# Performance work log

Hardware: AMD Instinct MI355X
Metric: run time of the kernel (lower is better)

## Reference

```python
import jax, jax.numpy as jnp
import numpy as np

N = 50000          # num nodes
E = 800000         # num edges
IN_C, HID_C, OUT_C = 128, 256, 256
LN_EPS = 1e-5


def gcn_conv(x, W, b, row, col):
    """PyG GCNConv: h = D^{-1/2}(A+I)D^{-1/2} (x W) + b, self-loops added."""
    h = x @ W                                             # [N, C_out]
    deg = jax.ops.segment_sum(jnp.ones((row.shape[0],), h.dtype), col,
                              num_segments=N) + 1.0        # +1 for self-loop
    dinv = jax.lax.rsqrt(deg)                              # [N]
    msg = h[row] * (dinv[row] * dinv[col])[:, None]        # [E, C_out] gathered msgs
    agg = jax.ops.segment_sum(msg, col, num_segments=N)
    agg = agg + h * (dinv * dinv)[:, None]                 # self-loop contribution
    return agg + b


def layer_norm(x, gamma, beta):
    mu = jnp.mean(x, axis=-1, keepdims=True)
    var = jnp.mean(jnp.square(x - mu), axis=-1, keepdims=True)
    return (x - mu) * jax.lax.rsqrt(var + LN_EPS) * gamma + beta


def setup_inputs() -> dict:
    key = jax.random.key(0)
    ks = jax.random.split(key, 8)
    x = jax.random.normal(ks[0], (N, IN_C), jnp.float32)
    edge_index = jax.random.randint(ks[1], (2, E), 0, N, dtype=jnp.int64)
    W1 = jax.random.normal(ks[2], (IN_C, HID_C), jnp.float32) * (1.0 / np.sqrt(IN_C))
    b1 = jnp.zeros((HID_C,), jnp.float32)
    W2 = jax.random.normal(ks[3], (HID_C, OUT_C), jnp.float32) * (1.0 / np.sqrt(HID_C))
    b2 = jnp.zeros((OUT_C,), jnp.float32)
    ln1_g = jnp.ones((HID_C,), jnp.float32); ln1_b = jnp.zeros((HID_C,), jnp.float32)
    ln2_g = jnp.ones((OUT_C,), jnp.float32); ln2_b = jnp.zeros((OUT_C,), jnp.float32)
    proj_W = jax.random.normal(ks[4], (IN_C, OUT_C), jnp.float32) * (1.0 / np.sqrt(IN_C))
    proj_b = jnp.zeros((OUT_C,), jnp.float32)
    return {"x": x, "edge_index": edge_index, "W1": W1, "b1": b1, "W2": W2,
            "b2": b2, "ln1_g": ln1_g, "ln1_b": ln1_b, "ln2_g": ln2_g,
            "ln2_b": ln2_b, "proj_W": proj_W, "proj_b": proj_b}


def reference(x, edge_index, W1, b1, W2, b2, ln1_g, ln1_b, ln2_g, ln2_b,
              proj_W, proj_b):
    row, col = edge_index[0], edge_index[1]   # messages flow row -> col
    identity = x @ proj_W + proj_b            # self.proj (Linear, in != out)
    h = gcn_conv(x, W1, b1, row, col)
    h = jax.nn.relu(layer_norm(h, ln1_g, ln1_b))   # dropout = identity (eval)
    g = gcn_conv(h, W2, b2, row, col)
    g = layer_norm(g, ln2_g, ln2_b)
    return jax.nn.relu(g + identity)
```

## Files before the change

### kernel.cpp

```cpp
#include <hip/hip_runtime.h>

#define NN 50000
#define NE 800000
#define LN_EPS 1e-5f

using bf16x8 = __attribute__((ext_vector_type(8))) short;
using f32x4  = __attribute__((ext_vector_type(4))) float;

__device__ __forceinline__ float b2f(unsigned short u) {
    union { unsigned int i; float f; } c;
    c.i = ((unsigned int)u) << 16;
    return c.f;
}
__device__ __forceinline__ unsigned short f2b(float f) {
    union { float f; unsigned int i; } c;
    c.f = f;
    const unsigned int i = c.i;
    return (unsigned short)((i + 0x7FFFu + ((i >> 16) & 1u)) >> 16);
}

__global__ __launch_bounds__(256) void cvt_k(const float* __restrict__ X,
                                             short* __restrict__ Xb, int n4) {
    const int i = blockIdx.x * 256 + threadIdx.x;
    if (i >= n4) return;
    const float4 v = ((const float4*)X)[i];
    ushort4 o;
    o.x = f2b(v.x); o.y = f2b(v.y); o.z = f2b(v.z); o.w = f2b(v.w);
    ((ushort4*)Xb)[i] = o;
}

template <int K>
__global__ __launch_bounds__(256) void pack_w_k(const float* __restrict__ W,
                                                short* __restrict__ Wp) {
    constexpr int KB = K / 32;
    const int i = blockIdx.x * 256 + threadIdx.x;
    const int j = i & 7;
    const int l = (i >> 3) & 63;
    const int t = i >> 9;
    const int kb = t % KB;
    const int nt = t / KB;
    const int k = 32 * kb + 8 * (l >> 4) + j;
    const int n = 16 * nt + (l & 15);
    Wp[i] = (short)f2b(W[(size_t)k * 256 + n]);
}

template <int K, bool OUT_BF16>
__global__ __launch_bounds__(256) void gemm_mfma_k(const short* __restrict__ X,
                                                   const short* __restrict__ Wp,
                                                   const float* __restrict__ bias,
                                                   void* __restrict__ Yv) {
    constexpr int KB = K / 32;
    const int lane = threadIdx.x & 63;
    const int wv = threadIdx.x >> 6;
    const int row0 = blockIdx.x * 64 + wv * 16;
    const int r = row0 + (lane & 15);
    const int rc = (r < NN) ? r : (NN - 1);
    const int kof = 8 * (lane >> 4);

    bf16x8 a[KB];
#pragma unroll
    for (int kb = 0; kb < KB; ++kb)
        a[kb] = *(const bf16x8*)(X + (size_t)rc * K + 32 * kb + kof);

    const int orow0 = row0 + (lane >> 4) * 4;
    const int colbase = lane & 15;

    for (int nt = 0; nt < 16; ++nt) {
        f32x4 acc = {0.f, 0.f, 0.f, 0.f};
#pragma unroll
        for (int kb = 0; kb < KB; ++kb) {
            const bf16x8 b = ((const bf16x8*)Wp)[(nt * KB + kb) * 64 + lane];
            acc = __builtin_amdgcn_mfma_f32_16x16x32_bf16(a[kb], b, acc, 0, 0, 0);
        }
        const int col = nt * 16 + colbase;
        const float bv = bias ? bias[col] : 0.f;
#pragma unroll
        for (int rg = 0; rg < 4; ++rg) {
            const int orow = orow0 + rg;
            if (orow < NN) {
                const float v = acc[rg] + bv;
                if (OUT_BF16)
                    ((short*)Yv)[(size_t)orow * 256 + col] = (short)f2b(v);
                else
                    ((float*)Yv)[(size_t)orow * 256 + col] = v;
            }
        }
    }
}

__global__ __launch_bounds__(256) void count_k(const int* __restrict__ col,
                                               int* __restrict__ rowptr) {
    const int e = blockIdx.x * 256 + threadIdx.x;
    if (e < NE) atomicAdd(&rowptr[col[e] + 1], 1);
}

__global__ __launch_bounds__(256) void block_sum_k(const int* __restrict__ p,
                                                   int* __restrict__ psum, int n) {
    __shared__ int sh[256];
    const int t = threadIdx.x;
    const int i = blockIdx.x * 256 + t;
    sh[t] = (i < n) ? p[i] : 0;
    __syncthreads();
#pragma unroll
    for (int off = 128; off > 0; off >>= 1) {
        if (t < off) sh[t] += sh[t + off];
        __syncthreads();
    }
    if (t == 0) psum[blockIdx.x] = sh[0];
}

__global__ __launch_bounds__(256) void scan_apply_k(int* __restrict__ p,
                                                    const int* __restrict__ psum,
                                                    int n, int nblk) {
    __shared__ int sh[256];
    const int t = threadIdx.x;
    const int b = blockIdx.x;
    const int i = b * 256 + t;
    sh[t] = (t < b && t < nblk) ? psum[t] : 0;
    __syncthreads();
#pragma unroll
    for (int off = 128; off > 0; off >>= 1) {
        if (t < off) sh[t] += sh[t + off];
        __syncthreads();
    }
    const int carry = sh[0];
    __syncthreads();
    sh[t] = (i < n) ? p[i] : 0;
    __syncthreads();
#pragma unroll
    for (int off = 1; off < 256; off <<= 1) {
        const int u = (t >= off) ? sh[t - off] : 0;
        __syncthreads();
        sh[t] += u;
        __syncthreads();
    }
    if (i < n) p[i] = sh[t] + carry;
}

__global__ __launch_bounds__(256) void dinv_k(const int* __restrict__ rowptr,
                                              float* __restrict__ dinv) {
    const int i = blockIdx.x * 256 + threadIdx.x;
    if (i < NN) dinv[i] = rsqrtf((float)(rowptr[i + 1] - rowptr[i]) + 1.0f);
}

__global__ __launch_bounds__(256) void fill_k(const int* __restrict__ row,
                                              const int* __restrict__ col,
                                              int* __restrict__ rowptr,
                                              int* __restrict__ srcs) {
    const int e = blockIdx.x * 256 + threadIdx.x;
    if (e >= NE) return;
    const int pos = atomicAdd(&rowptr[col[e]], 1);
    srcs[pos] = row[e];
}

template <bool OUT_BF16>
__global__ __launch_bounds__(256) void gather_post_k(
    const short* __restrict__ H, const int* __restrict__ endptr,
    const int* __restrict__ srcs, const float* __restrict__ dinv,
    const float* __restrict__ bias, const float* __restrict__ gamma,
    const float* __restrict__ beta, const float* __restrict__ resid,
    void* __restrict__ outv) {
    const int node = blockIdx.x * 4 + (threadIdx.x >> 6);
    const int lane = threadIdx.x & 63;
    if (node >= NN) return;
    const int start = node ? endptr[node - 1] : 0;
    const int end = endptr[node];

    float a0 = 0.f, a1 = 0.f, a2 = 0.f, a3 = 0.f;
    int j = start;
    for (; j + 1 < end; j += 2) {
        const int r0 = srcs[j];
        const int r1 = srcs[j + 1];
        const float w0 = dinv[r0];
        const float w1 = dinv[r1];
        const ushort4 v0 = ((const ushort4*)(H + (size_t)r0 * 256))[lane];
        const ushort4 v1 = ((const ushort4*)(H + (size_t)r1 * 256))[lane];
        a0 += b2f(v0.x) * w0 + b2f(v1.x) * w1;
        a1 += b2f(v0.y) * w0 + b2f(v1.y) * w1;
        a2 += b2f(v0.z) * w0 + b2f(v1.z) * w1;
        a3 += b2f(v0.w) * w0 + b2f(v1.w) * w1;
    }
    if (j < end) {
        const int r0 = srcs[j];
        const float w0 = dinv[r0];
        const ushort4 v0 = ((const ushort4*)(H + (size_t)r0 * 256))[lane];
        a0 += b2f(v0.x) * w0;
        a1 += b2f(v0.y) * w0;
        a2 += b2f(v0.z) * w0;
        a3 += b2f(v0.w) * w0;
    }

    const float dc = dinv[node];
    const ushort4 h = ((const ushort4*)(H + (size_t)node * 256))[lane];
    const float4 b = ((const float4*)bias)[lane];
    float t0 = (a0 + b2f(h.x) * dc) * dc + b.x;
    float t1 = (a1 + b2f(h.y) * dc) * dc + b.y;
    float t2 = (a2 + b2f(h.z) * dc) * dc + b.z;
    float t3 = (a3 + b2f(h.w) * dc) * dc + b.w;

    float s = t0 + t1 + t2 + t3;
    float q = t0 * t0 + t1 * t1 + t2 * t2 + t3 * t3;
#pragma unroll
    for (int off = 1; off < 64; off <<= 1) {
        s += __shfl_xor(s, off, 64);
        q += __shfl_xor(q, off, 64);
    }
    const float mu = s * (1.f / 256.f);
    const float var = q * (1.f / 256.f) - mu * mu;
    const float rs = rsqrtf(var + LN_EPS);

    const float4 g = ((const float4*)gamma)[lane];
    const float4 be = ((const float4*)beta)[lane];
    t0 = (t0 - mu) * rs * g.x + be.x;
    t1 = (t1 - mu) * rs * g.y + be.y;
    t2 = (t2 - mu) * rs * g.z + be.z;
    t3 = (t3 - mu) * rs * g.w + be.w;

    if (resid) {
        const float4 rv = ((const float4*)(resid + (size_t)node * 256))[lane];
        t0 += rv.x; t1 += rv.y; t2 += rv.z; t3 += rv.w;
    }
    t0 = fmaxf(t0, 0.f); t1 = fmaxf(t1, 0.f);
    t2 = fmaxf(t2, 0.f); t3 = fmaxf(t3, 0.f);

    if (OUT_BF16) {
        ushort4 o;
        o.x = f2b(t0); o.y = f2b(t1); o.z = f2b(t2); o.w = f2b(t3);
        ((ushort4*)outv)[(size_t)node * 64 + lane] = o;
    } else {
        float4 o;
        o.x = t0; o.y = t1; o.z = t2; o.w = t3;
        ((float4*)outv)[(size_t)node * 64 + lane] = o;
    }
}

extern "C" void kernel_launch(void* const* d_in, const int* in_sizes, int n_in,
                              void* d_out, int out_size, void* d_ws, size_t ws_size,
                              hipStream_t stream) {
    const float* x    = (const float*)d_in[0];
    const int*   eidx = (const int*)d_in[1];
    const float* W1   = (const float*)d_in[2];
    const float* b1   = (const float*)d_in[3];
    const float* W2   = (const float*)d_in[4];
    const float* b2   = (const float*)d_in[5];
    const float* ln1g = (const float*)d_in[6];
    const float* ln1b = (const float*)d_in[7];
    const float* ln2g = (const float*)d_in[8];
    const float* ln2b = (const float*)d_in[9];
    const float* pW   = (const float*)d_in[10];
    const float* pb   = (const float*)d_in[11];

    const int* row = eidx;
    const int* col = eidx + NE;
    float* out = (float*)d_out;

    short* xb     = (short*)d_ws;
    short* A      = xb + (size_t)NN * 128;
    short* Bb     = A + (size_t)NN * 256;
    float* dinv   = (float*)(Bb + (size_t)NN * 256);
    int*   rowptr = (int*)(dinv + NN);
    int*   psum   = rowptr + NN + 4;
    int*   srcs   = psum + 256;
    short* Wp1    = (short*)(srcs + NE);
    short* Wp2    = Wp1 + 128 * 256;
    short* Wpp    = Wp2 + 256 * 256;

    const int nscan = NN + 1;
    const int nblk = (nscan + 255) / 256;

    cvt_k<<<(NN * 128 / 4 + 255) / 256, 256, 0, stream>>>(x, xb, NN * 128 / 4);
    pack_w_k<128><<<128, 256, 0, stream>>>(W1, Wp1);
    pack_w_k<256><<<256, 256, 0, stream>>>(W2, Wp2);
    pack_w_k<128><<<128, 256, 0, stream>>>(pW, Wpp);

    hipMemsetAsync(rowptr, 0, (NN + 4) * sizeof(int), stream);
    count_k<<<(NE + 255) / 256, 256, 0, stream>>>(col, rowptr);
    block_sum_k<<<nblk, 256, 0, stream>>>(rowptr, psum, nscan);
    scan_apply_k<<<nblk, 256, 0, stream>>>(rowptr, psum, nscan, nblk);
    dinv_k<<<(NN + 255) / 256, 256, 0, stream>>>(rowptr, dinv);
    fill_k<<<(NE + 255) / 256, 256, 0, stream>>>(row, col, rowptr, srcs);

    gemm_mfma_k<128, true><<<(NN + 63) / 64, 256, 0, stream>>>(xb, Wp1, nullptr, A);
    gather_post_k<true><<<(NN + 3) / 4, 256, 0, stream>>>(A, rowptr, srcs, dinv,
                                                          b1, ln1g, ln1b, nullptr, Bb);

    gemm_mfma_k<128, false><<<(NN + 63) / 64, 256, 0, stream>>>(xb, Wpp, pb, out);

    gemm_mfma_k<256, true><<<(NN + 63) / 64, 256, 0, stream>>>(Bb, Wp2, nullptr, A);
    gather_post_k<false><<<(NN + 3) / 4, 256, 0, stream>>>(A, rowptr, srcs, dinv,
                                                           b2, ln2g, ln2b, out, out);
}
```

Baseline: 331.9 us.

## Aggregate before transform and fuse GEMM with bias, LayerNorm and projection

Reorders each GCN layer to aggregate first and multiply by the weight afterwards, using linearity. Layer 1 then gathers 128-wide rows of x instead of 256-wide rows of xW. LayerNorm, bias, the residual projection GEMM and ReLU move into the GEMM epilogue, removing the separate projection pass and the fp32 out read-modify-write. In exchange the GEMM keeps 16 accumulator tiles per wave, which raises register pressure and may lower occupancy. Rounding also shifts because aggregated values are rounded to bf16 before the matmul.

```diff
diff --git a/kernel.cpp b/kernel.cpp
--- a/kernel.cpp
+++ b/kernel.cpp
@@ -44,50 +44,6 @@
     Wp[i] = (short)f2b(W[(size_t)k * 256 + n]);
 }
 
-template <int K, bool OUT_BF16>
-__global__ __launch_bounds__(256) void gemm_mfma_k(const short* __restrict__ X,
-                                                   const short* __restrict__ Wp,
-                                                   const float* __restrict__ bias,
-                                                   void* __restrict__ Yv) {
-    constexpr int KB = K / 32;
-    const int lane = threadIdx.x & 63;
-    const int wv = threadIdx.x >> 6;
-    const int row0 = blockIdx.x * 64 + wv * 16;
-    const int r = row0 + (lane & 15);
-    const int rc = (r < NN) ? r : (NN - 1);
-    const int kof = 8 * (lane >> 4);
-
-    bf16x8 a[KB];
-#pragma unroll
-    for (int kb = 0; kb < KB; ++kb)
-        a[kb] = *(const bf16x8*)(X + (size_t)rc * K + 32 * kb + kof);
-
-    const int orow0 = row0 + (lane >> 4) * 4;
-    const int colbase = lane & 15;
-
-    for (int nt = 0; nt < 16; ++nt) {
-        f32x4 acc = {0.f, 0.f, 0.f, 0.f};
-#pragma unroll
-        for (int kb = 0; kb < KB; ++kb) {
-            const bf16x8 b = ((const bf16x8*)Wp)[(nt * KB + kb) * 64 + lane];
-            acc = __builtin_amdgcn_mfma_f32_16x16x32_bf16(a[kb], b, acc, 0, 0, 0);
-        }
-        const int col = nt * 16 + colbase;
-        const float bv = bias ? bias[col] : 0.f;
-#pragma unroll
-        for (int rg = 0; rg < 4; ++rg) {
-            const int orow = orow0 + rg;
-            if (orow < NN) {
-                const float v = acc[rg] + bv;
-                if (OUT_BF16)
-                    ((short*)Yv)[(size_t)orow * 256 + col] = (short)f2b(v);
-                else
-                    ((float*)Yv)[(size_t)orow * 256 + col] = v;
-            }
-        }
-    }
-}
-
 __global__ __launch_bounds__(256) void count_k(const int* __restrict__ col,
                                                int* __restrict__ rowptr) {
     const int e = blockIdx.x * 256 + threadIdx.x;
@@ -153,13 +109,50 @@
     srcs[pos] = row[e];
 }
 
-template <bool OUT_BF16>
-__global__ __launch_bounds__(256) void gather_post_k(
-    const short* __restrict__ H, const int* __restrict__ endptr,
-    const int* __restrict__ srcs, const float* __restrict__ dinv,
-    const float* __restrict__ bias, const float* __restrict__ gamma,
-    const float* __restrict__ beta, const float* __restrict__ resid,
-    void* __restrict__ outv) {
+__global__ __launch_bounds__(256) void gather1_k(const short* __restrict__ X,
+                                                 const int* __restrict__ endptr,
+                                                 const int* __restrict__ srcs,
+                                                 const float* __restrict__ dinv,
+                                                 short* __restrict__ A1) {
+    const int node = blockIdx.x * 4 + (threadIdx.x >> 6);
+    const int lane = threadIdx.x & 63;
+    if (node >= NN) return;
+    const int start = node ? endptr[node - 1] : 0;
+    const int end = endptr[node];
+
+    float a0 = 0.f, a1 = 0.f;
+    int j = start;
+    for (; j + 1 < end; j += 2) {
+        const int r0 = srcs[j];
+        const int r1 = srcs[j + 1];
+        const float w0 = dinv[r0];
+        const float w1 = dinv[r1];
+        const ushort2 v0 = ((const ushort2*)(X + (size_t)r0 * 128))[lane];
+        const ushort2 v1 = ((const ushort2*)(X + (size_t)r1 * 128))[lane];
+        a0 += b2f(v0.x) * w0 + b2f(v1.x) * w1;
+        a1 += b2f(v0.y) * w0 + b2f(v1.y) * w1;
+    }
+    if (j < end) {
+        const int r0 = srcs[j];
+        const float w0 = dinv[r0];
+        const ushort2 v0 = ((const ushort2*)(X + (size_t)r0 * 128))[lane];
+        a0 += b2f(v0.x) * w0;
+        a1 += b2f(v0.y) * w0;
+    }
+    const float dc = dinv[node];
+    const ushort2 h = ((const ushort2*)(X + (size_t)node * 128))[lane];
+    a0 = (a0 + b2f(h.x) * dc) * dc;
+    a1 = (a1 + b2f(h.y) * dc) * dc;
+    ushort2 o;
+    o.x = f2b(a0); o.y = f2b(a1);
+    ((ushort2*)A1)[(size_t)node * 64 + lane] = o;
+}
+
+__global__ __launch_bounds__(256) void gather2_k(const short* __restrict__ H,
+                                                 const int* __restrict__ endptr,
+                                                 const int* __restrict__ srcs,
+                                                 const float* __restrict__ dinv,
+                                                 short* __restrict__ agg) {
     const int node = blockIdx.x * 4 + (threadIdx.x >> 6);
     const int lane = threadIdx.x & 63;
     if (node >= NN) return;
@@ -189,48 +182,114 @@
         a2 += b2f(v0.z) * w0;
         a3 += b2f(v0.w) * w0;
     }
-
     const float dc = dinv[node];
     const ushort4 h = ((const ushort4*)(H + (size_t)node * 256))[lane];
-    const float4 b = ((const float4*)bias)[lane];
-    float t0 = (a0 + b2f(h.x) * dc) * dc + b.x;
-    float t1 = (a1 + b2f(h.y) * dc) * dc + b.y;
-    float t2 = (a2 + b2f(h.z) * dc) * dc + b.z;
-    float t3 = (a3 + b2f(h.w) * dc) * dc + b.w;
-
-    float s = t0 + t1 + t2 + t3;
-    float q = t0 * t0 + t1 * t1 + t2 * t2 + t3 * t3;
-#pragma unroll
-    for (int off = 1; off < 64; off <<= 1) {
-        s += __shfl_xor(s, off, 64);
-        q += __shfl_xor(q, off, 64);
-    }
-    const float mu = s * (1.f / 256.f);
-    const float var = q * (1.f / 256.f) - mu * mu;
-    const float rs = rsqrtf(var + LN_EPS);
-
-    const float4 g = ((const float4*)gamma)[lane];
-    const float4 be = ((const float4*)beta)[lane];
-    t0 = (t0 - mu) * rs * g.x + be.x;
-    t1 = (t1 - mu) * rs * g.y + be.y;
-    t2 = (t2 - mu) * rs * g.z + be.z;
-    t3 = (t3 - mu) * rs * g.w + be.w;
-
-    if (resid) {
-        const float4 rv = ((const float4*)(resid + (size_t)node * 256))[lane];
-        t0 += rv.x; t1 += rv.y; t2 += rv.z; t3 += rv.w;
-    }
-    t0 = fmaxf(t0, 0.f); t1 = fmaxf(t1, 0.f);
-    t2 = fmaxf(t2, 0.f); t3 = fmaxf(t3, 0.f);
-
-    if (OUT_BF16) {
-        ushort4 o;
-        o.x = f2b(t0); o.y = f2b(t1); o.z = f2b(t2); o.w = f2b(t3);
-        ((ushort4*)outv)[(size_t)node * 64 + lane] = o;
-    } else {
-        float4 o;
-        o.x = t0; o.y = t1; o.z = t2; o.w = t3;
-        ((float4*)outv)[(size_t)node * 64 + lane] = o;
+    ushort4 o;
+    o.x = f2b((a0 + b2f(h.x) * dc) * dc);
+    o.y = f2b((a1 + b2f(h.y) * dc) * dc);
+    o.z = f2b((a2 + b2f(h.z) * dc) * dc);
+    o.w = f2b((a3 + b2f(h.w) * dc) * dc);
+    ((ushort4*)agg)[(size_t)node * 64 + lane] = o;
+}
+
+template <int K, bool PROJ, bool OUT_BF16>
+__global__ __launch_bounds__(256) void gemm_ln_k(
+    const short* __restrict__ X, const short* __restrict__ Wp,
+    const float* __restrict__ bias, const float* __restrict__ gamma,
+    const float* __restrict__ beta, const short* __restrict__ Xp,
+    const short* __restrict__ Wpp, const float* __restrict__ pbias,
+    void* __restrict__ Yv) {
+    constexpr int KB = K / 32;
+    const int lane = threadIdx.x & 63;
+    const int wv = threadIdx.x >> 6;
+    const int row0 = blockIdx.x * 64 + wv * 16;
+    const int r = row0 + (lane & 15);
+    const int rc = (r < NN) ? r : (NN - 1);
+    const int kof = 8 * (lane >> 4);
+    const int colbase = lane & 15;
+
+    bf16x8 a[KB];
+#pragma unroll
+    for (int kb = 0; kb < KB; ++kb)
+        a[kb] = *(const bf16x8*)(X + (size_t)rc * K + 32 * kb + kof);
+
+    f32x4 acc[16];
+#pragma unroll
+    for (int nt = 0; nt < 16; ++nt) {
+        f32x4 c = {0.f, 0.f, 0.f, 0.f};
+#pragma unroll
+        for (int kb = 0; kb < KB; ++kb) {
+            const bf16x8 b = ((const bf16x8*)Wp)[(nt * KB + kb) * 64 + lane];
+            c = __builtin_amdgcn_mfma_f32_16x16x32_bf16(a[kb], b, c, 0, 0, 0);
+        }
+        acc[nt] = c;
+    }
+
+    float s[4] = {0.f, 0.f, 0.f, 0.f};
+    float q[4] = {0.f, 0.f, 0.f, 0.f};
+#pragma unroll
+    for (int nt = 0; nt < 16; ++nt) {
+        const float bv = bias[nt * 16 + colbase];
+#pragma unroll
+        for (int rg = 0; rg < 4; ++rg) {
+            const float v = acc[nt][rg] + bv;
+            acc[nt][rg] = v;
+            s[rg] += v;
+            q[rg] += v * v;
+        }
+    }
+#pragma unroll
+    for (int off = 1; off < 16; off <<= 1) {
+#pragma unroll
+        for (int rg = 0; rg < 4; ++rg) {
+            s[rg] += __shfl_xor(s[rg], off, 64);
+            q[rg] += __shfl_xor(q[rg], off, 64);
+        }
+    }
+    float mu[4], rsd[4];
+#pragma unroll
+    for (int rg = 0; rg < 4; ++rg) {
+        mu[rg] = s[rg] * (1.f / 256.f);
+        const float var = q[rg] * (1.f / 256.f) - mu[rg] * mu[rg];
+        rsd[rg] = rsqrtf(var + LN_EPS);
+    }
+
+    bf16x8 ap[4];
+    if (PROJ) {
+#pragma unroll
+        for (int kb = 0; kb < 4; ++kb)
+            ap[kb] = *(const bf16x8*)(Xp + (size_t)rc * 128 + 32 * kb + kof);
+    }
+
+    const int orow0 = row0 + (lane >> 4) * 4;
+#pragma unroll
+    for (int nt = 0; nt < 16; ++nt) {
+        const int col = nt * 16 + colbase;
+        const float g = gamma[col];
+        const float be = beta[col];
+        f32x4 pid = {0.f, 0.f, 0.f, 0.f};
+        float pbv = 0.f;
+        if (PROJ) {
+#pragma unroll
+            for (int kb = 0; kb < 4; ++kb) {
+                const bf16x8 b = ((const bf16x8*)Wpp)[(nt * 4 + kb) * 64 + lane];
+                pid = __builtin_amdgcn_mfma_f32_16x16x32_bf16(ap[kb], b, pid, 0, 0, 0);
+            }
+            pbv = pbias[col];
+        }
+#pragma unroll
+        for (int rg = 0; rg < 4; ++rg) {
+            const int orow = orow0 + rg;
+            float v = (acc[nt][rg] - mu[rg]) * rsd[rg] * g + be;
+            if (PROJ) v += pid[rg] + pbv;
+            v = fmaxf(v, 0.f);
+            if (orow < NN) {
+                if (OUT_BF16)
+                    ((short*)Yv)[(size_t)orow * 256 + col] = (short)f2b(v);
+                else
+                    ((float*)Yv)[(size_t)orow * 256 + col] = v;
+            }
+        }
     }
 }
 
@@ -255,9 +314,10 @@
     float* out = (float*)d_out;
 
     short* xb     = (short*)d_ws;
-    short* A      = xb + (size_t)NN * 128;
-    short* Bb     = A + (size_t)NN * 256;
-    float* dinv   = (float*)(Bb + (size_t)NN * 256);
+    short* A1     = xb + (size_t)NN * 128;
+    short* Bb     = A1 + (size_t)NN * 128;
+    short* Ag     = Bb + (size_t)NN * 256;
+    float* dinv   = (float*)(Ag + (size_t)NN * 256);
     int*   rowptr = (int*)(dinv + NN);
     int*   psum   = rowptr + NN + 4;
     int*   srcs   = psum + 256;
@@ -280,13 +340,11 @@
     dinv_k<<<(NN + 255) / 256, 256, 0, stream>>>(rowptr, dinv);
     fill_k<<<(NE + 255) / 256, 256, 0, stream>>>(row, col, rowptr, srcs);
 
-    gemm_mfma_k<128, true><<<(NN + 63) / 64, 256, 0, stream>>>(xb, Wp1, nullptr, A);
-    gather_post_k<true><<<(NN + 3) / 4, 256, 0, stream>>>(A, rowptr, srcs, dinv,
-                                                          b1, ln1g, ln1b, nullptr, Bb);
-
-    gemm_mfma_k<128, false><<<(NN + 63) / 64, 256, 0, stream>>>(xb, Wpp, pb, out);
-
-    gemm_mfma_k<256, true><<<(NN + 63) / 64, 256, 0, stream>>>(Bb, Wp2, nullptr, A);
-    gather_post_k<false><<<(NN + 3) / 4, 256, 0, stream>>>(A, rowptr, srcs, dinv,
-                                                           b2, ln2g, ln2b, out, out);
-}
+    gather1_k<<<(NN + 3) / 4, 256, 0, stream>>>(xb, rowptr, srcs, dinv, A1);
+    gemm_ln_k<128, false, true><<<(NN + 63) / 64, 256, 0, stream>>>(
+        A1, Wp1, b1, ln1g, ln1b, nullptr, nullptr, nullptr, Bb);
+
+    gather2_k<<<(NN + 3) / 4, 256, 0, stream>>>(Bb, rowptr, srcs, dinv, Ag);
+    gemm_ln_k<256, true, false><<<(NN + 63) / 64, 256, 0, stream>>>(
+        Ag, Wp2, b2, ln2g, ln2b, xb, Wpp, pb, out);
+}
```

New measurement: 379.9 us. 1.14x slower.
